# Performance work log

Hardware: AMD Instinct MI355X
Metric: run time of the kernel (lower is better)

The kernel has to match this reference:

```python
import jax, jax.numpy as jnp
import numpy as np

D_MODEL, N_HEAD, D_HEAD, D_ROPE = 2048, 16, 128, 64
D_KV, D_Q = 512, 1024
THETA = 10000.0


def _cos_sin(seq_len):
    # freqs_cis equivalent: angles [seq_len, d_rope//2]
    inv = 1.0 / (THETA ** (jnp.arange(0, D_ROPE, 2, dtype=jnp.float32) / D_ROPE))
    ang = jnp.arange(seq_len, dtype=jnp.float32)[:, None] * inv[None, :]
    return jnp.cos(ang), jnp.sin(ang)


def _rope(t, cos, sin):
    # t: [b, s, h, d_rope]; rotate interleaved (even, odd) pairs as complex mult
    t1, t2 = t[..., 0::2], t[..., 1::2]
    c = cos[None, :, None, :]
    s = sin[None, :, None, :]
    out = jnp.stack([t1 * c - t2 * s, t1 * s + t2 * c], axis=-1)
    return out.reshape(t.shape)


def setup_inputs() -> dict:
    key = jax.random.key(0)
    ks = jax.random.split(key, 10)
    b, s = 1, 2048
    x = jax.random.normal(ks[0], (b, s, D_MODEL), dtype=jnp.float32)
    # additive causal mask [s, s]
    mask = jnp.where(jnp.tril(jnp.ones((s, s), dtype=bool)), 0.0, -1e9).astype(jnp.float32)
    def w(k, fan_in, fan_out):
        lim = (6.0 / (fan_in + fan_out)) ** 0.5  # xavier_uniform
        return jax.random.uniform(k, (fan_in, fan_out), jnp.float32, -lim, lim)
    return {
        'x': x, 'mask': mask,
        'W_kv_down': w(ks[1], D_MODEL, D_KV),
        'W_k_up':    w(ks[2], D_KV, N_HEAD * D_HEAD),
        'W_v_up':    w(ks[3], D_KV, N_HEAD * D_HEAD),
        'W_q_down':  w(ks[4], D_MODEL, D_Q),
        'W_q_up':    w(ks[5], D_Q, N_HEAD * D_HEAD),
        'W_q_rope':  w(ks[6], D_Q, N_HEAD * D_ROPE),
        'W_k_rope':  w(ks[7], D_MODEL, N_HEAD * D_ROPE),
        'W_out':     w(ks[8], N_HEAD * D_HEAD, D_MODEL),
    }


def reference(x, mask, W_kv_down, W_k_up, W_v_up, W_q_down, W_q_up, W_q_rope, W_k_rope, W_out):
    b, s, _ = x.shape
    cos, sin = _cos_sin(s)
    # low-rank KV path
    down_kv = x @ W_kv_down                                      # [b,s,d_kv]
    k_c = (down_kv @ W_k_up).reshape(b, s, N_HEAD, D_HEAD)
    v   = (down_kv @ W_v_up).reshape(b, s, N_HEAD, D_HEAD)
    # low-rank Q path
    down_q = x @ W_q_down                                        # [b,s,d_q]
    q_c = (down_q @ W_q_up).reshape(b, s, N_HEAD, D_HEAD)
    q_r = (down_q @ W_q_rope).reshape(b, s, N_HEAD, D_ROPE)
    k_r = (x @ W_k_rope).reshape(b, s, N_HEAD, D_ROPE)
    # decoupled RoPE on rope parts only
    q_r = _rope(q_r, cos, sin)
    k_r = _rope(k_r, cos, sin)
    # concat content + rope, heads to dim 1
    q = jnp.concatenate([q_c, q_r], axis=-1).transpose(0, 2, 1, 3)  # [b,h,s,dh+dr]
    k = jnp.concatenate([k_c, k_r], axis=-1).transpose(0, 2, 1, 3)
    vv = v.transpose(0, 2, 1, 3)                                     # [b,h,s,dh]
    scale = 1.0 / jnp.sqrt(jnp.float32(D_HEAD + D_ROPE))
    scores = jnp.einsum('bhqd,bhkd->bhqk', q, k) * scale + mask[None, None]
    probs = jax.nn.softmax(scores.astype(jnp.float32), axis=-1).astype(q.dtype)
    out = jnp.einsum('bhqk,bhkd->bhqd', probs, vv)                   # [b,h,s,dh]
    out = out.transpose(0, 2, 1, 3).reshape(b, s, N_HEAD * D_HEAD)
    return out @ W_out
```

## Files before the change

kernel.cpp:

```cpp
#include <hip/hip_runtime.h>
#include <hip/hip_bf16.h>
#include <math.h>

#define S 2048
#define DM 2048
#define NH 16
#define DH 128
#define DR 64
#define DKV 512
#define DQ 1024
#define DQK 192
#define QSCALE 0.07216878364870323f

typedef __bf16 bf16x8 __attribute__((ext_vector_type(8)));
typedef float f32x4 __attribute__((ext_vector_type(4)));
typedef unsigned short u16;

__device__ inline unsigned int pack2_bf16(float a, float b) {
    __hip_bfloat16 ha = __float2bfloat16(a);
    __hip_bfloat16 hb = __float2bfloat16(b);
    unsigned short ua = *reinterpret_cast<unsigned short*>(&ha);
    unsigned short ub = *reinterpret_cast<unsigned short*>(&hb);
    return (unsigned int)ua | ((unsigned int)ub << 16);
}
__device__ inline u16 f2bf(float v) {
    __hip_bfloat16 hb = __float2bfloat16(v);
    return *reinterpret_cast<u16*>(&hb);
}
__device__ inline void gload_lds16(const void* g, void* l) {
    __builtin_amdgcn_global_load_lds(
        (const __attribute__((address_space(1))) void*)g,
        (__attribute__((address_space(3))) void*)l, 16, 0, 0);
}

__global__ __launch_bounds__(256) void prep_kernel(
    const float* __restrict__ x,
    const float* __restrict__ W0, const float* __restrict__ W1, const float* __restrict__ W2,
    const float* __restrict__ W3, const float* __restrict__ W4, const float* __restrict__ W5,
    const float* __restrict__ W6, const float* __restrict__ W7,
    u16* __restrict__ x_bf,
    u16* __restrict__ D0, u16* __restrict__ D1, u16* __restrict__ D2, u16* __restrict__ D3,
    u16* __restrict__ D4, u16* __restrict__ D5, u16* __restrict__ D6, u16* __restrict__ D7,
    float* __restrict__ cosT, float* __restrict__ sinT) {
    __shared__ u16 tile[64][65];
    const int b = blockIdx.x;
    if (b < 3584) {
        const float* W; u16* D; int N, K, local;
        if (b < 256)       { W = W0; D = D0; N = 512;  K = 2048; local = b; }
        else if (b < 768)  { W = W1; D = D1; N = 1024; K = 2048; local = b - 256; }
        else if (b < 1280) { W = W2; D = D2; N = 1024; K = 2048; local = b - 768; }
        else if (b < 1536) { W = W3; D = D3; N = 2048; K = 512;  local = b - 1280; }
        else if (b < 1792) { W = W4; D = D4; N = 2048; K = 512;  local = b - 1536; }
        else if (b < 2304) { W = W5; D = D5; N = 2048; K = 1024; local = b - 1792; }
        else if (b < 2560) { W = W6; D = D6; N = 1024; K = 1024; local = b - 2304; }
        else               { W = W7; D = D7; N = 2048; K = 2048; local = b - 2560; }
        const int nt = N / 64;
        const int n0 = (local % nt) * 64;
        const int k0 = (local / nt) * 64;
        const int tx = threadIdx.x & 15;
        const int ty = threadIdx.x >> 4;
#pragma unroll
        for (int rep = 0; rep < 4; ++rep) {
            int kk = rep * 16 + ty;
            float4 v = *reinterpret_cast<const float4*>(&W[(size_t)(k0 + kk) * N + n0 + tx * 4]);
            tile[kk][tx * 4 + 0] = f2bf(v.x);
            tile[kk][tx * 4 + 1] = f2bf(v.y);
            tile[kk][tx * 4 + 2] = f2bf(v.z);
            tile[kk][tx * 4 + 3] = f2bf(v.w);
        }
        __syncthreads();
#pragma unroll
        for (int rep = 0; rep < 4; ++rep) {
            int nn = rep * 16 + ty;
            uint2 w;
            w.x = (unsigned int)tile[tx * 4 + 0][nn] | ((unsigned int)tile[tx * 4 + 1][nn] << 16);
            w.y = (unsigned int)tile[tx * 4 + 2][nn] | ((unsigned int)tile[tx * 4 + 3][nn] << 16);
            *reinterpret_cast<uint2*>(&D[(size_t)(n0 + nn) * K + k0 + tx * 4]) = w;
        }
    } else if (b < 7680) {
        int idx = (b - 3584) * 256 + threadIdx.x;
        float4 v = *reinterpret_cast<const float4*>(&x[(size_t)idx * 4]);
        uint2 w;
        w.x = pack2_bf16(v.x, v.y);
        w.y = pack2_bf16(v.z, v.w);
        *reinterpret_cast<uint2*>(&x_bf[(size_t)idx * 4]) = w;
    } else {
        int idx = (b - 7680) * 256 + threadIdx.x;
        int pos = idx / (DR / 2);
        int j   = idx % (DR / 2);
        float inv = __expf(-((float)(2 * j) / (float)DR) * logf(10000.0f));
        float ang = (float)pos * inv;
        cosT[idx] = cosf(ang);
        sinT[idx] = sinf(ang);
    }
}

template <int MODE>
__device__ __forceinline__ void gemm_core(
    u16 (*lds)[6144],
    const u16* __restrict__ A, const u16* __restrict__ BT,
    void* __restrict__ P0v, void* __restrict__ P1v, void* __restrict__ P2v,
    const float* __restrict__ cosT, const float* __restrict__ sinT, int K,
    int bm, int bn) {
    const int tid  = threadIdx.x;
    const int wave = tid >> 6;
    const int lane = tid & 63;
    const int c16  = lane & 15;
    const int g    = lane >> 4;
    const int wm = (wave >> 1) * 32;
    const int wn = (wave & 1) * 64;

    f32x4 acc[2][4];
#pragma unroll
    for (int i = 0; i < 2; ++i)
#pragma unroll
        for (int j = 0; j < 4; ++j) acc[i][j] = f32x4{0.f, 0.f, 0.f, 0.f};

    auto stage = [&](int buf, int k0) {
        {
            int L = tid;
            int rp = L >> 3, e = L & 7, x = e ^ (rp & 7);
            int row = 2 * rp + (x >> 2), kc = x & 3;
            gload_lds16(A + (size_t)(bm + row) * K + k0 + kc * 8, &lds[buf][wave * 512]);
        }
#pragma unroll
        for (int r = 0; r < 2; ++r) {
            int L = r * 256 + tid;
            int rp = L >> 3, e = L & 7, x = e ^ (rp & 7);
            int row = 2 * rp + (x >> 2), kc = x & 3;
            gload_lds16(BT + (size_t)(bn + row) * K + k0 + kc * 8,
                        &lds[buf][2048 + (r * 256 + wave * 64) * 8]);
        }
    };

    const int NT = K / 32;
    stage(0, 0);
    __syncthreads();
    int cur = 0;
    for (int t = 0; t < NT; ++t) {
        if (t + 1 < NT) stage(cur ^ 1, (t + 1) * 32);
        bf16x8 af[2], bfr[4];
#pragma unroll
        for (int i = 0; i < 2; ++i) {
            int row  = wm + i * 16 + c16;
            int slot = ((row >> 1) << 3) + ((((row & 1) << 2) + g) ^ ((row >> 1) & 7));
            af[i] = *reinterpret_cast<const bf16x8*>(&lds[cur][slot * 8]);
        }
#pragma unroll
        for (int j = 0; j < 4; ++j) {
            int row  = wn + j * 16 + c16;
            int slot = ((row >> 1) << 3) + ((((row & 1) << 2) + g) ^ ((row >> 1) & 7));
            bfr[j] = *reinterpret_cast<const bf16x8*>(&lds[cur][2048 + slot * 8]);
        }
#pragma unroll
        for (int i = 0; i < 2; ++i)
#pragma unroll
            for (int j = 0; j < 4; ++j)
                acc[i][j] = __builtin_amdgcn_mfma_f32_16x16x32_bf16(af[i], bfr[j], acc[i][j], 0, 0, 0);
        __syncthreads();
        cur ^= 1;
    }

#pragma unroll
    for (int i = 0; i < 2; ++i)
#pragma unroll
        for (int j = 0; j < 4; ++j) {
            const int mrow = bm + wm + i * 16 + g * 4;
            const int col  = bn + wn + j * 16 + c16;
            if constexpr (MODE == 0) {
                if (col < 512) {
                    u16* down_kv = (u16*)P0v;
#pragma unroll
                    for (int r = 0; r < 4; ++r)
                        down_kv[(size_t)(mrow + r) * DKV + col] = f2bf(acc[i][j][r]);
                } else if (col < 1536) {
                    u16* down_q = (u16*)P1v;
#pragma unroll
                    for (int r = 0; r < 4; ++r)
                        down_q[(size_t)(mrow + r) * DQ + (col - 512)] = f2bf(acc[i][j][r]);
                } else {
                    u16* k_asm = (u16*)P2v;
                    const int cc = col - 1536, h = cc >> 6, rr = cc & 63, jj = rr >> 1;
#pragma unroll
                    for (int r = 0; r < 4; ++r) {
                        int pos = mrow + r;
                        float self = acc[i][j][r];
                        float vp   = __shfl_xor(self, 1);
                        float c = cosT[pos * (DR / 2) + jj];
                        float s = sinT[pos * (DR / 2) + jj];
                        float val = (rr & 1) ? (vp * s + self * c) : (self * c - vp * s);
                        k_asm[((size_t)h * S + pos) * DQK + DH + rr] = f2bf(val);
                    }
                }
            } else if constexpr (MODE == 1) {
                if (col < 2048) {
                    u16* k_asm = (u16*)P0v;
                    const int h = col >> 7, d = col & 127;
#pragma unroll
                    for (int r = 0; r < 4; ++r)
                        k_asm[((size_t)h * S + mrow + r) * DQK + d] = f2bf(acc[i][j][r]);
                } else {
                    u16* vt = (u16*)P1v;
                    const int cc = col - 2048, h = cc >> 7, d = cc & 127;
                    uint2 w;
                    w.x = pack2_bf16(acc[i][j][0], acc[i][j][1]);
                    w.y = pack2_bf16(acc[i][j][2], acc[i][j][3]);
                    *reinterpret_cast<uint2*>(&vt[((size_t)h * DH + d) * S + mrow]) = w;
                }
            } else if constexpr (MODE == 2) {
                u16* q_asm = (u16*)P0v;
                if (col < 2048) {
                    const int h = col >> 7, d = col & 127;
#pragma unroll
                    for (int r = 0; r < 4; ++r)
                        q_asm[((size_t)h * S + mrow + r) * DQK + d] = f2bf(acc[i][j][r] * QSCALE);
                } else {
                    const int cc = col - 2048, h = cc >> 6, rr = cc & 63, jj = rr >> 1;
#pragma unroll
                    for (int r = 0; r < 4; ++r) {
                        int pos = mrow + r;
                        float self = acc[i][j][r];
                        float vp   = __shfl_xor(self, 1);
                        float c = cosT[pos * (DR / 2) + jj];
                        float s = sinT[pos * (DR / 2) + jj];
                        float val = (rr & 1) ? (vp * s + self * c) : (self * c - vp * s);
                        q_asm[((size_t)h * S + pos) * DQK + DH + rr] = f2bf(val * QSCALE);
                    }
                }
            } else {
                float* outp = (float*)P0v;
#pragma unroll
                for (int r = 0; r < 4; ++r)
                    outp[(size_t)(mrow + r) * DM + col] = acc[i][j][r];
            }
        }
}

template <int MODE>
__global__ __launch_bounds__(256) void gemm_fused_kernel(
    const u16* __restrict__ A, const u16* __restrict__ BT,
    void* __restrict__ P0v, void* __restrict__ P1v, void* __restrict__ P2v,
    const float* __restrict__ cosT, const float* __restrict__ sinT, int K) {
    __shared__ u16 lds[2][6144];
    gemm_core<MODE>(lds, A, BT, P0v, P1v, P2v, cosT, sinT, K,
                    blockIdx.y * 64, blockIdx.x * 128);
}

__global__ __launch_bounds__(256) void gemm_g23_kernel(
    const u16* __restrict__ down_kv, const u16* __restrict__ WT2,
    const u16* __restrict__ down_q,  const u16* __restrict__ WT3,
    u16* __restrict__ k_asm, u16* __restrict__ vt, u16* __restrict__ q_asm,
    const float* __restrict__ cosT, const float* __restrict__ sinT) {
    __shared__ u16 lds[2][6144];
    const int b = blockIdx.x;
    if (b < 1024) {
        gemm_core<1>(lds, down_kv, WT2, k_asm, vt, nullptr, cosT, sinT, DKV,
                     (b >> 5) * 64, (b & 31) * 128);
    } else {
        const int l = b - 1024;
        gemm_core<2>(lds, down_q, WT3, q_asm, nullptr, nullptr, cosT, sinT, DQ,
                     (l / 24) * 64, (l % 24) * 128);
    }
}

__global__ __launch_bounds__(256) void attn_mfma_kernel(const u16* __restrict__ q,
                                                        const u16* __restrict__ k,
                                                        const u16* __restrict__ vt,
                                                        u16* __restrict__ outp) {
    const int wgid = blockIdx.x;
    const int xcd  = wgid & 7;
    const int i    = wgid >> 3;
    const int h  = (i < 32) ? (xcd * 2) : (xcd * 2 + 1);
    const int qt = (i < 32) ? (31 - i) : (i - 32);
    const int q0 = qt * 64;

    const int tid  = threadIdx.x;
    const int wave = tid >> 6;
    const int lane = tid & 63;
    const int col  = lane & 15;
    const int g    = lane >> 4;
    const int qw   = q0 + wave * 16;

    __shared__ u16 Kt[2][32 * DQK];
    __shared__ u16 Vt[2][DH * 32];
    __shared__ __align__(16) u16 p_lds[4][512];

    const int r7  = col & 7;
    const int pv7 = (col >> 1) & 7;
    const int pvb = (col & 1) << 2;

    bf16x8 qf[6];
    const u16* qbase = q + ((size_t)h * S + qw + col) * DQK + g * 8;
#pragma unroll
    for (int c = 0; c < 6; ++c) qf[c] = *reinterpret_cast<const bf16x8*>(qbase + c * 32);

    f32x4 acc[8];
#pragma unroll
    for (int c = 0; c < 8; ++c) acc[c] = f32x4{0.f, 0.f, 0.f, 0.f};
    float m_run = -1e30f, l_run = 0.f;

    auto stage = [&](int buf, int j0) {
#pragma unroll
        for (int r = 0; r < 3; ++r) {
            int L   = r * 256 + tid;
            int row = L / 24, rem = L - row * 24;
            int ch  = ((rem >> 3) << 3) + ((rem & 7) ^ (row & 7));
            gload_lds16(k + ((size_t)h * S + j0 + row) * DQK + ch * 8,
                        &Kt[buf][(r * 256 + wave * 64) * 8]);
        }
#pragma unroll
        for (int r = 0; r < 2; ++r) {
            int L  = r * 256 + tid;
            int rp = L >> 3, x = (L & 7) ^ (rp & 7);
            int d  = 2 * rp + (x >> 2), kc = x & 3;
            gload_lds16(vt + ((size_t)h * DH + d) * S + j0 + kc * 8,
                        &Vt[buf][(r * 256 + wave * 64) * 8]);
        }
    };

    const int kend = q0 + 64;
    stage(0, 0);
    __syncthreads();
    int cur = 0;
    for (int j0 = 0; j0 < kend; j0 += 32) {
        if (j0 + 32 < kend) stage(cur ^ 1, j0 + 32);
        f32x4 st[2];
        st[0] = f32x4{0.f, 0.f, 0.f, 0.f};
        st[1] = f32x4{0.f, 0.f, 0.f, 0.f};
#pragma unroll
        for (int t = 0; t < 2; ++t) {
            int rb = (16 * t + col) * 24;
#pragma unroll
            for (int c = 0; c < 6; ++c) {
                int ch   = g + 4 * c;
                int slot = rb + ((ch >> 3) << 3) + ((ch & 7) ^ r7);
                bf16x8 kf = *reinterpret_cast<const bf16x8*>(&Kt[cur][slot * 8]);
                st[t] = __builtin_amdgcn_mfma_f32_16x16x32_bf16(kf, qf[c], st[t], 0, 0, 0);
            }
        }
#pragma unroll
        for (int t = 0; t < 2; ++t) {
            if (j0 + 16 * t + 15 > qw) {
#pragma unroll
                for (int r = 0; r < 4; ++r) {
                    int key = j0 + 16 * t + 4 * g + r;
                    st[t][r] = (key > qw + col) ? -1e30f : st[t][r];
                }
            }
        }
        float tmax = fmaxf(fmaxf(fmaxf(st[0][0], st[0][1]), fmaxf(st[0][2], st[0][3])),
                           fmaxf(fmaxf(st[1][0], st[1][1]), fmaxf(st[1][2], st[1][3])));
        tmax = fmaxf(tmax, __shfl_xor(tmax, 16));
        tmax = fmaxf(tmax, __shfl_xor(tmax, 32));
        float m_new;
        if (__all(tmax - m_run <= 8.0f)) {
            m_new = m_run;
        } else {
            m_new = fmaxf(m_run, tmax);
            float r_scale = __expf(m_run - m_new);
            l_run *= r_scale;
#pragma unroll
            for (int c = 0; c < 8; ++c) {
                acc[c][0] *= r_scale; acc[c][1] *= r_scale;
                acc[c][2] *= r_scale; acc[c][3] *= r_scale;
            }
            m_run = m_new;
        }
        float p[8];
        float psum = 0.f;
#pragma unroll
        for (int t = 0; t < 2; ++t)
#pragma unroll
            for (int r = 0; r < 4; ++r) {
                float pv = __expf(st[t][r] - m_new);
                p[t * 4 + r] = pv;
                psum += pv;
            }
        psum += __shfl_xor(psum, 16);
        psum += __shfl_xor(psum, 32);
        l_run += psum;
#pragma unroll
        for (int t = 0; t < 2; ++t) {
            uint2 w;
            w.x = pack2_bf16(p[t * 4 + 0], p[t * 4 + 1]);
            w.y = pack2_bf16(p[t * 4 + 2], p[t * 4 + 3]);
            int ch   = 2 * t + (g >> 1);
            int slot = ((col >> 1) << 3) + ((pvb + ch) ^ pv7);
            *reinterpret_cast<uint2*>(&p_lds[wave][slot * 8 + (g & 1) * 4]) = w;
        }
        {
            int slot = ((col >> 1) << 3) + ((pvb + g) ^ pv7);
            bf16x8 pf = *reinterpret_cast<const bf16x8*>(&p_lds[wave][slot * 8]);
#pragma unroll
            for (int c = 0; c < 8; ++c) {
                int d  = 16 * c + col;
                int vs = ((d >> 1) << 3) + ((pvb + g) ^ pv7);
                bf16x8 vf = *reinterpret_cast<const bf16x8*>(&Vt[cur][vs * 8]);
                acc[c] = __builtin_amdgcn_mfma_f32_16x16x32_bf16(vf, pf, acc[c], 0, 0, 0);
            }
        }
        __syncthreads();
        cur ^= 1;
    }

    float inv_l = 1.0f / l_run;
#pragma unroll
    for (int c = 0; c < 8; ++c)
#pragma unroll
        for (int r = 0; r < 4; ++r)
            outp[(size_t)(qw + col) * (NH * DH) + h * DH + 16 * c + 4 * g + r] = f2bf(acc[c][r] * inv_l);
}

extern "C" void kernel_launch(void* const* d_in, const int* in_sizes, int n_in,
                              void* d_out, int out_size, void* d_ws, size_t ws_size,
                              hipStream_t stream) {
    const float* x         = (const float*)d_in[0];
    const float* W_kv_down = (const float*)d_in[2];
    const float* W_k_up    = (const float*)d_in[3];
    const float* W_v_up    = (const float*)d_in[4];
    const float* W_q_down  = (const float*)d_in[5];
    const float* W_q_up    = (const float*)d_in[6];
    const float* W_q_rope  = (const float*)d_in[7];
    const float* W_k_rope  = (const float*)d_in[8];
    const float* W_out     = (const float*)d_in[9];
    float* out = (float*)d_out;

    float* w = (float*)d_ws;
    float* cosT = w;
    float* sinT = w + (size_t)S * (DR / 2);
    u16* b = (u16*)(w + 2 * (size_t)S * (DR / 2));
    size_t off = 0;
    u16* x_bf    = b + off; off += (size_t)S * DM;
    u16* WT1     = b + off; off += (size_t)2560 * DM;
    u16* WT2     = b + off; off += (size_t)4096 * DKV;
    u16* WT3     = b + off; off += (size_t)3072 * DQ;
    u16* WT4     = b + off; off += (size_t)DM * DM;
    u16* down_kv = b + off; off += (size_t)S * DKV;
    u16* down_q  = b + off; off += (size_t)S * DQ;
    u16* q_asm   = b + off; off += (size_t)NH * S * DQK;
    u16* k_asm   = b + off; off += (size_t)NH * S * DQK;
    u16* vt      = b + off; off += (size_t)NH * DH * S;
    u16* attn_bf = b + off; off += (size_t)S * NH * DH;

    prep_kernel<<<7936, 256, 0, stream>>>(
        x, W_kv_down, W_q_down, W_k_rope, W_k_up, W_v_up, W_q_up, W_q_rope, W_out,
        x_bf,
        WT1, WT1 + (size_t)512 * DM, WT1 + (size_t)1536 * DM,
        WT2, WT2 + (size_t)2048 * DKV,
        WT3, WT3 + (size_t)2048 * DQ, WT4,
        cosT, sinT);

    gemm_fused_kernel<0><<<dim3(2560 / 128, S / 64), 256, 0, stream>>>(
        x_bf, WT1, down_kv, down_q, k_asm, cosT, sinT, DM);

    gemm_g23_kernel<<<1792, 256, 0, stream>>>(
        down_kv, WT2, down_q, WT3, k_asm, vt, q_asm, cosT, sinT);

    attn_mfma_kernel<<<512, 256, 0, stream>>>(q_asm, k_asm, vt, attn_bf);

    gemm_fused_kernel<3><<<dim3(DM / 128, S / 64), 256, 0, stream>>>(
        attn_bf, WT4, out, nullptr, nullptr, cosT, sinT, DM);
}
```

Before: 213.6 us.

## Triple-buffer K/V tiles with explicit vmcnt waits and one barrier per iteration

The attention loop moves from double to triple buffering of K and V tiles in LDS. Loads are issued two tiles ahead, and each iteration starts with an s_waitcnt vmcnt that waits only for the oldest tile, then a single barrier. The trailing __syncthreads is gone. This is meant to hide global load latency and halve barrier count, at the cost of more LDS per block (which may reduce occupancy) and correctness that depends on exact vmcnt counts for the async LDS loads.

```diff
diff --git a/kernel.cpp b/kernel.cpp
--- a/kernel.cpp
+++ b/kernel.cpp
@@ -281,8 +281,8 @@
     const int g    = lane >> 4;
     const int qw   = q0 + wave * 16;
 
-    __shared__ u16 Kt[2][32 * DQK];
-    __shared__ u16 Vt[2][DH * 32];
+    __shared__ u16 Kt[3][32 * DQK];
+    __shared__ u16 Vt[3][DH * 32];
     __shared__ __align__(16) u16 p_lds[4][512];
 
     const int r7  = col & 7;
@@ -318,33 +318,40 @@
         }
     };
 
-    const int kend = q0 + 64;
+    const int T = 2 * qt + 2;
     stage(0, 0);
-    __syncthreads();
-    int cur = 0;
-    for (int j0 = 0; j0 < kend; j0 += 32) {
-        if (j0 + 32 < kend) stage(cur ^ 1, j0 + 32);
+    if (T > 1) stage(1, 32);
+
+    for (int t = 0; t < T; ++t) {
+        if (t + 1 < T) asm volatile("s_waitcnt vmcnt(5)" ::: "memory");
+        else           asm volatile("s_waitcnt vmcnt(0)" ::: "memory");
+        __builtin_amdgcn_s_barrier();
+        asm volatile("" ::: "memory");
+        if (t + 2 < T) stage((t + 2) % 3, (t + 2) * 32);
+        const int cur = t % 3;
+        const int j0  = t * 32;
+
         f32x4 st[2];
         st[0] = f32x4{0.f, 0.f, 0.f, 0.f};
         st[1] = f32x4{0.f, 0.f, 0.f, 0.f};
 #pragma unroll
-        for (int t = 0; t < 2; ++t) {
-            int rb = (16 * t + col) * 24;
+        for (int tt = 0; tt < 2; ++tt) {
+            int rb = (16 * tt + col) * 24;
 #pragma unroll
             for (int c = 0; c < 6; ++c) {
                 int ch   = g + 4 * c;
                 int slot = rb + ((ch >> 3) << 3) + ((ch & 7) ^ r7);
                 bf16x8 kf = *reinterpret_cast<const bf16x8*>(&Kt[cur][slot * 8]);
-                st[t] = __builtin_amdgcn_mfma_f32_16x16x32_bf16(kf, qf[c], st[t], 0, 0, 0);
-            }
-        }
-#pragma unroll
-        for (int t = 0; t < 2; ++t) {
-            if (j0 + 16 * t + 15 > qw) {
+                st[tt] = __builtin_amdgcn_mfma_f32_16x16x32_bf16(kf, qf[c], st[tt], 0, 0, 0);
+            }
+        }
+#pragma unroll
+        for (int tt = 0; tt < 2; ++tt) {
+            if (j0 + 16 * tt + 15 > qw) {
 #pragma unroll
                 for (int r = 0; r < 4; ++r) {
-                    int key = j0 + 16 * t + 4 * g + r;
-                    st[t][r] = (key > qw + col) ? -1e30f : st[t][r];
+                    int key = j0 + 16 * tt + 4 * g + r;
+                    st[tt][r] = (key > qw + col) ? -1e30f : st[tt][r];
                 }
             }
         }
@@ -369,22 +376,22 @@
         float p[8];
         float psum = 0.f;
 #pragma unroll
-        for (int t = 0; t < 2; ++t)
+        for (int tt = 0; tt < 2; ++tt)
 #pragma unroll
             for (int r = 0; r < 4; ++r) {
-                float pv = __expf(st[t][r] - m_new);
-                p[t * 4 + r] = pv;
+                float pv = __expf(st[tt][r] - m_new);
+                p[tt * 4 + r] = pv;
                 psum += pv;
             }
         psum += __shfl_xor(psum, 16);
         psum += __shfl_xor(psum, 32);
         l_run += psum;
 #pragma unroll
-        for (int t = 0; t < 2; ++t) {
+        for (int tt = 0; tt < 2; ++tt) {
             uint2 w;
-            w.x = pack2_bf16(p[t * 4 + 0], p[t * 4 + 1]);
-            w.y = pack2_bf16(p[t * 4 + 2], p[t * 4 + 3]);
-            int ch   = 2 * t + (g >> 1);
+            w.x = pack2_bf16(p[tt * 4 + 0], p[tt * 4 + 1]);
+            w.y = pack2_bf16(p[tt * 4 + 2], p[tt * 4 + 3]);
+            int ch   = 2 * tt + (g >> 1);
             int slot = ((col >> 1) << 3) + ((pvb + ch) ^ pv7);
             *reinterpret_cast<uint2*>(&p_lds[wave][slot * 8 + (g & 1) * 4]) = w;
         }
@@ -399,8 +406,6 @@
                 acc[c] = __builtin_amdgcn_mfma_f32_16x16x32_bf16(vf, pf, acc[c], 0, 0, 0);
             }
         }
-        __syncthreads();
-        cur ^= 1;
     }
 
     float inv_l = 1.0f / l_run;
```

Result: slower. 219.2 us (+2.6%).

## Process two 16-row query groups per wave in attention, halving block size

Applied to the files above, without the earlier changes.

The attention kernel now runs 2 waves (128 threads) per 64-query tile instead of 4, with each wave handling 32 query rows as two 16-row groups. Each K and V fragment read from LDS is reused for two MFMAs, which halves LDS read traffic per MFMA and lets independent MFMAs interleave. The cost is higher register pressure (two Q fragment sets, two accumulator sets) and fewer waves per block to hide latency, with each thread issuing twice as many staging loads.

```diff
diff --git a/kernel.cpp b/kernel.cpp
--- a/kernel.cpp
+++ b/kernel.cpp
@@ -263,7 +263,7 @@
     }
 }
 
-__global__ __launch_bounds__(256) void attn_mfma_kernel(const u16* __restrict__ q,
+__global__ __launch_bounds__(128) void attn_mfma_kernel(const u16* __restrict__ q,
                                                         const u16* __restrict__ k,
                                                         const u16* __restrict__ vt,
                                                         u16* __restrict__ outp) {
@@ -279,42 +279,47 @@
     const int lane = tid & 63;
     const int col  = lane & 15;
     const int g    = lane >> 4;
-    const int qw   = q0 + wave * 16;
+    const int qw   = q0 + wave * 32;
 
     __shared__ u16 Kt[2][32 * DQK];
     __shared__ u16 Vt[2][DH * 32];
-    __shared__ __align__(16) u16 p_lds[4][512];
+    __shared__ __align__(16) u16 p_lds[2][2][512];
 
     const int r7  = col & 7;
     const int pv7 = (col >> 1) & 7;
     const int pvb = (col & 1) << 2;
 
-    bf16x8 qf[6];
-    const u16* qbase = q + ((size_t)h * S + qw + col) * DQK + g * 8;
-#pragma unroll
-    for (int c = 0; c < 6; ++c) qf[c] = *reinterpret_cast<const bf16x8*>(qbase + c * 32);
-
-    f32x4 acc[8];
-#pragma unroll
-    for (int c = 0; c < 8; ++c) acc[c] = f32x4{0.f, 0.f, 0.f, 0.f};
-    float m_run = -1e30f, l_run = 0.f;
+    bf16x8 qf[2][6];
+#pragma unroll
+    for (int grp = 0; grp < 2; ++grp) {
+        const u16* qbase = q + ((size_t)h * S + qw + grp * 16 + col) * DQK + g * 8;
+#pragma unroll
+        for (int c = 0; c < 6; ++c) qf[grp][c] = *reinterpret_cast<const bf16x8*>(qbase + c * 32);
+    }
+
+    f32x4 acc[2][8];
+#pragma unroll
+    for (int grp = 0; grp < 2; ++grp)
+#pragma unroll
+        for (int c = 0; c < 8; ++c) acc[grp][c] = f32x4{0.f, 0.f, 0.f, 0.f};
+    float m_run[2] = {-1e30f, -1e30f}, l_run[2] = {0.f, 0.f};
 
     auto stage = [&](int buf, int j0) {
 #pragma unroll
-        for (int r = 0; r < 3; ++r) {
-            int L   = r * 256 + tid;
+        for (int r = 0; r < 6; ++r) {
+            int L   = r * 128 + tid;
             int row = L / 24, rem = L - row * 24;
             int ch  = ((rem >> 3) << 3) + ((rem & 7) ^ (row & 7));
             gload_lds16(k + ((size_t)h * S + j0 + row) * DQK + ch * 8,
-                        &Kt[buf][(r * 256 + wave * 64) * 8]);
-        }
-#pragma unroll
-        for (int r = 0; r < 2; ++r) {
-            int L  = r * 256 + tid;
+                        &Kt[buf][(r * 128 + wave * 64) * 8]);
+        }
+#pragma unroll
+        for (int r = 0; r < 4; ++r) {
+            int L  = r * 128 + tid;
             int rp = L >> 3, x = (L & 7) ^ (rp & 7);
             int d  = 2 * rp + (x >> 2), kc = x & 3;
             gload_lds16(vt + ((size_t)h * DH + d) * S + j0 + kc * 8,
-                        &Vt[buf][(r * 256 + wave * 64) * 8]);
+                        &Vt[buf][(r * 128 + wave * 64) * 8]);
         }
     };
 
@@ -324,91 +329,103 @@
     int cur = 0;
     for (int j0 = 0; j0 < kend; j0 += 32) {
         if (j0 + 32 < kend) stage(cur ^ 1, j0 + 32);
-        f32x4 st[2];
-        st[0] = f32x4{0.f, 0.f, 0.f, 0.f};
-        st[1] = f32x4{0.f, 0.f, 0.f, 0.f};
-#pragma unroll
-        for (int t = 0; t < 2; ++t) {
-            int rb = (16 * t + col) * 24;
+        f32x4 st[2][2];
+#pragma unroll
+        for (int grp = 0; grp < 2; ++grp)
+#pragma unroll
+            for (int tt = 0; tt < 2; ++tt) st[grp][tt] = f32x4{0.f, 0.f, 0.f, 0.f};
+#pragma unroll
+        for (int tt = 0; tt < 2; ++tt) {
+            int rb = (16 * tt + col) * 24;
 #pragma unroll
             for (int c = 0; c < 6; ++c) {
                 int ch   = g + 4 * c;
                 int slot = rb + ((ch >> 3) << 3) + ((ch & 7) ^ r7);
                 bf16x8 kf = *reinterpret_cast<const bf16x8*>(&Kt[cur][slot * 8]);
-                st[t] = __builtin_amdgcn_mfma_f32_16x16x32_bf16(kf, qf[c], st[t], 0, 0, 0);
+                st[0][tt] = __builtin_amdgcn_mfma_f32_16x16x32_bf16(kf, qf[0][c], st[0][tt], 0, 0, 0);
+                st[1][tt] = __builtin_amdgcn_mfma_f32_16x16x32_bf16(kf, qf[1][c], st[1][tt], 0, 0, 0);
             }
         }
-#pragma unroll
-        for (int t = 0; t < 2; ++t) {
-            if (j0 + 16 * t + 15 > qw) {
+        bf16x8 pf[2];
+#pragma unroll
+        for (int grp = 0; grp < 2; ++grp) {
+            const int qrow = qw + grp * 16 + col;
+            const int qwg  = qw + grp * 16;
+#pragma unroll
+            for (int tt = 0; tt < 2; ++tt) {
+                if (j0 + 16 * tt + 15 > qwg) {
+#pragma unroll
+                    for (int r = 0; r < 4; ++r) {
+                        int key = j0 + 16 * tt + 4 * g + r;
+                        st[grp][tt][r] = (key > qrow) ? -1e30f : st[grp][tt][r];
+                    }
+                }
+            }
+            float tmax = fmaxf(fmaxf(fmaxf(st[grp][0][0], st[grp][0][1]), fmaxf(st[grp][0][2], st[grp][0][3])),
+                               fmaxf(fmaxf(st[grp][1][0], st[grp][1][1]), fmaxf(st[grp][1][2], st[grp][1][3])));
+            tmax = fmaxf(tmax, __shfl_xor(tmax, 16));
+            tmax = fmaxf(tmax, __shfl_xor(tmax, 32));
+            float m_new;
+            if (__all(tmax - m_run[grp] <= 8.0f)) {
+                m_new = m_run[grp];
+            } else {
+                m_new = fmaxf(m_run[grp], tmax);
+                float r_scale = __expf(m_run[grp] - m_new);
+                l_run[grp] *= r_scale;
+#pragma unroll
+                for (int c = 0; c < 8; ++c) {
+                    acc[grp][c][0] *= r_scale; acc[grp][c][1] *= r_scale;
+                    acc[grp][c][2] *= r_scale; acc[grp][c][3] *= r_scale;
+                }
+                m_run[grp] = m_new;
+            }
+            float p[8];
+            float psum = 0.f;
+#pragma unroll
+            for (int tt = 0; tt < 2; ++tt)
 #pragma unroll
                 for (int r = 0; r < 4; ++r) {
-                    int key = j0 + 16 * t + 4 * g + r;
-                    st[t][r] = (key > qw + col) ? -1e30f : st[t][r];
-                }
+                    float pv = __expf(st[grp][tt][r] - m_new);
+                    p[tt * 4 + r] = pv;
+                    psum += pv;
+                }
+            psum += __shfl_xor(psum, 16);
+            psum += __shfl_xor(psum, 32);
+            l_run[grp] += psum;
+#pragma unroll
+            for (int tt = 0; tt < 2; ++tt) {
+                uint2 w;
+                w.x = pack2_bf16(p[tt * 4 + 0], p[tt * 4 + 1]);
+                w.y = pack2_bf16(p[tt * 4 + 2], p[tt * 4 + 3]);
+                int ch   = 2 * tt + (g >> 1);
+                int slot = ((col >> 1) << 3) + ((pvb + ch) ^ pv7);
+                *reinterpret_cast<uint2*>(&p_lds[wave][grp][slot * 8 + (g & 1) * 4]) = w;
             }
-        }
-        float tmax = fmaxf(fmaxf(fmaxf(st[0][0], st[0][1]), fmaxf(st[0][2], st[0][3])),
-                           fmaxf(fmaxf(st[1][0], st[1][1]), fmaxf(st[1][2], st[1][3])));
-        tmax = fmaxf(tmax, __shfl_xor(tmax, 16));
-        tmax = fmaxf(tmax, __shfl_xor(tmax, 32));
-        float m_new;
-        if (__all(tmax - m_run <= 8.0f)) {
-            m_new = m_run;
-        } else {
-            m_new = fmaxf(m_run, tmax);
-            float r_scale = __expf(m_run - m_new);
-            l_run *= r_scale;
-#pragma unroll
-            for (int c = 0; c < 8; ++c) {
-                acc[c][0] *= r_scale; acc[c][1] *= r_scale;
-                acc[c][2] *= r_scale; acc[c][3] *= r_scale;
-            }
-            m_run = m_new;
-        }
-        float p[8];
-        float psum = 0.f;
-#pragma unroll
-        for (int t = 0; t < 2; ++t)
-#pragma unroll
-            for (int r = 0; r < 4; ++r) {
-                float pv = __expf(st[t][r] - m_new);
-                p[t * 4 + r] = pv;
-                psum += pv;
-            }
-        psum += __shfl_xor(psum, 16);
-        psum += __shfl_xor(psum, 32);
-        l_run += psum;
-#pragma unroll
-        for (int t = 0; t < 2; ++t) {
-            uint2 w;
-            w.x = pack2_bf16(p[t * 4 + 0], p[t * 4 + 1]);
-            w.y = pack2_bf16(p[t * 4 + 2], p[t * 4 + 3]);
-            int ch   = 2 * t + (g >> 1);
-            int slot = ((col >> 1) << 3) + ((pvb + ch) ^ pv7);
-            *reinterpret_cast<uint2*>(&p_lds[wave][slot * 8 + (g & 1) * 4]) = w;
-        }
-        {
             int slot = ((col >> 1) << 3) + ((pvb + g) ^ pv7);
-            bf16x8 pf = *reinterpret_cast<const bf16x8*>(&p_lds[wave][slot * 8]);
-#pragma unroll
-            for (int c = 0; c < 8; ++c) {
-                int d  = 16 * c + col;
-                int vs = ((d >> 1) << 3) + ((pvb + g) ^ pv7);
-                bf16x8 vf = *reinterpret_cast<const bf16x8*>(&Vt[cur][vs * 8]);
-                acc[c] = __builtin_amdgcn_mfma_f32_16x16x32_bf16(vf, pf, acc[c], 0, 0, 0);
-            }
+            pf[grp] = *reinterpret_cast<const bf16x8*>(&p_lds[wave][grp][slot * 8]);
+        }
+#pragma unroll
+        for (int c = 0; c < 8; ++c) {
+            int d  = 16 * c + col;
+            int vs = ((d >> 1) << 3) + ((pvb + g) ^ pv7);
+            bf16x8 vf = *reinterpret_cast<const bf16x8*>(&Vt[cur][vs * 8]);
+            acc[0][c] = __builtin_amdgcn_mfma_f32_16x16x32_bf16(vf, pf[0], acc[0][c], 0, 0, 0);
+            acc[1][c] = __builtin_amdgcn_mfma_f32_16x16x32_bf16(vf, pf[1], acc[1][c], 0, 0, 0);
         }
         __syncthreads();
         cur ^= 1;
     }
 
-    float inv_l = 1.0f / l_run;
-#pragma unroll
-    for (int c = 0; c < 8; ++c)
-#pragma unroll
-        for (int r = 0; r < 4; ++r)
-            outp[(size_t)(qw + col) * (NH * DH) + h * DH + 16 * c + 4 * g + r] = f2bf(acc[c][r] * inv_l);
+#pragma unroll
+    for (int grp = 0; grp < 2; ++grp) {
+        float inv_l = 1.0f / l_run[grp];
+#pragma unroll
+        for (int c = 0; c < 8; ++c)
+#pragma unroll
+            for (int r = 0; r < 4; ++r)
+                outp[(size_t)(qw + grp * 16 + col) * (NH * DH) + h * DH + 16 * c + 4 * g + r] =
+                    f2bf(acc[grp][c][r] * inv_l);
+    }
 }
 
 extern "C" void kernel_launch(void* const* d_in, const int* in_sizes, int n_in,
@@ -456,7 +473,7 @@
     gemm_g23_kernel<<<1792, 256, 0, stream>>>(
         down_kv, WT2, down_q, WT3, k_asm, vt, q_asm, cosT, sinT);
 
-    attn_mfma_kernel<<<512, 256, 0, stream>>>(q_asm, k_asm, vt, attn_bf);
+    attn_mfma_kernel<<<512, 128, 0, stream>>>(q_asm, k_asm, vt, attn_bf);
 
     gemm_fused_kernel<3><<<dim3(DM / 128, S / 64), 256, 0, stream>>>(
         attn_bf, WT4, out, nullptr, nullptr, cosT, sinT, DM);
```

Result: slower. 260.9 us (+22.1%).
